# Performance work log

Hardware: AMD Instinct MI355X
Metric: run time of the kernel (lower is better)

The kernel has to match this reference:

```python
import jax, jax.numpy as jnp
import numpy as np

NCLASSES = 80
MAX_BOXES = 100
IOU_THR = 0.5
SCORE_THR = 0.0
NEG = -1e9


def arrange_bbox(xy, wh):
    # xy, wh: [1, H, W, 3, 2]
    H, W = xy.shape[1], xy.shape[2]
    gx, gy = jnp.meshgrid(jnp.arange(W), jnp.arange(H))  # 'xy' indexing, each [H, W]
    grid = jnp.stack([gx, gy], axis=-1)[:, :, None, :].astype(xy.dtype)  # [H, W, 1, 2]
    gsize = jnp.array([H, W], dtype=xy.dtype)  # TF divides last dim [x, y] by [H, W]
    xy = (xy + grid) / gsize
    return jnp.concatenate([xy - wh / 2, xy + wh / 2], axis=-1)  # [1,H,W,3,4]


def hard_nms(boxes, scores):
    # boxes: [N,4] (x1,y1,x2,y2); scores: [N]. Greedy NMS, fixed MAX_BOXES output.
    areas = (boxes[:, 2] - boxes[:, 0]) * (boxes[:, 3] - boxes[:, 1])  # [N]

    def step(sw, _):
        j = jnp.argmax(sw)
        s = sw[j]
        valid = s > SCORE_THR
        bj = boxes[j]
        iw = jnp.clip(jnp.minimum(boxes[:, 2], bj[2]) - jnp.maximum(boxes[:, 0], bj[0]), 0.0)
        ih = jnp.clip(jnp.minimum(boxes[:, 3], bj[3]) - jnp.maximum(boxes[:, 1], bj[1]), 0.0)
        inter = iw * ih
        iou = inter / (areas + areas[j] - inter)
        sw = jnp.where((iou > IOU_THR) & valid, NEG, sw)  # suppresses j itself too
        return sw, (jnp.where(valid, j, -1), jnp.where(valid, s, 0.0), valid)

    _, (sel_idx, sel_scores, valids) = jax.lax.scan(step, scores, None, length=MAX_BOXES)
    return sel_idx, sel_scores, valids


def decode(grid0, grid1, grid2, anchors_table):
    outs = (grid0, grid1, grid2)
    anch = (anchors_table[2], anchors_table[1], anchors_table[0])
    bbs, confs, probs = [], [], []
    for g, a in zip(outs, anch):
        xy, wh, obj, cp = jnp.split(g, [2, 4, 5], axis=-1)
        b = arrange_bbox(xy, jnp.exp(wh) * a)
        bbs.append(b.reshape(1, -1, 4))
        confs.append(obj.reshape(1, -1, 1))
        probs.append(cp.reshape(1, -1, NCLASSES))
    bbox = jnp.concatenate(bbs, axis=1).reshape(-1, 4)          # [N,4]
    conf = jnp.concatenate(confs, axis=1)[0, :, 0]              # [N]
    cp = jnp.concatenate(probs, axis=1)[0]                      # [N,C]
    cls_idx = jnp.argmax(cp, axis=-1)                           # [N]
    maxprob = jnp.max(cp, axis=-1)                              # [N]
    # TF code broadcasts conf[1,N,1]*maxprob[N] -> [N,N], then reduce_max over axis 1.
    # Mathematically: scores[i] = max_j conf[i]*maxprob[j] = max(conf*max(mp), conf*min(mp)).
    scores = jnp.maximum(conf * jnp.max(maxprob), conf * jnp.min(maxprob))
    return bbox, scores, cls_idx


def reference(grid0, grid1, grid2, anchors_table):
    bbox, scores, cls_idx = decode(grid0, grid1, grid2, anchors_table)
    sel_idx, sel_scores, valids = hard_nms(bbox, scores)
    safe = jnp.clip(sel_idx, 0)
    sel_boxes = jnp.where(valids[:, None], bbox[safe], 0.0)[None]      # [1,MAX,4]
    sel_scores = sel_scores[None]                                       # [1,MAX]
    sel_classes = jnp.where(valids, cls_idx[safe], 0)[None]            # [1,MAX]
    num_valid = jnp.sum(valids).astype(jnp.int32)[None]                # [1]
    return sel_boxes, sel_scores, sel_classes, num_valid


def setup_inputs() -> dict:
    key = jax.random.key(0)
    k0, k1, k2 = jax.random.split(key, 3)
    grid0 = jax.random.normal(k0, (1, 48, 48, 3, 85), jnp.float32)
    grid1 = jax.random.normal(k1, (1, 96, 96, 3, 85), jnp.float32)
    grid2 = jax.random.normal(k2, (1, 192, 192, 3, 85), jnp.float32)
    anchors = np.array([[[10, 13], [16, 30], [33, 23]],
                        [[30, 61], [62, 45], [59, 119]],
                        [[116, 90], [156, 198], [373, 326]]], np.float32) / 416.0
    return {"grid0": grid0, "grid1": grid1, "grid2": grid2,
            "anchors_table": jnp.asarray(anchors)}
```

## Files before the change

### kernel.cpp

```cpp
#include <hip/hip_runtime.h>
#include <hip/hip_bf16.h>
#include <math.h>


#define NCLS  80
#define MAXB  100
#define N0    6912
#define N1    27648
#define NTOT  145152
#define NTILE 2268
#define NHB   567
#define NB    4096
#define CAP   2048
#define CAPL  2048
#define NEGF  -3.402823466e38f
#define POSF   3.402823466e38f

#define WS_CONF 0
#define WS_SCAL (NTOT * 4)
#define WS_PART (WS_SCAL + 16)
#define WS_HIST (WS_PART + NTILE * 16)
#define WS_BINC (WS_HIST + 8 * NB * 4)
#define WS_SUF  (WS_BINC + NB * 4)
#define WS_META (WS_SUF + (NB + 4) * 4)
#define WS_CAND (WS_META + 16)

__device__ __forceinline__ int binOf(float s, float Smax) {
    int b = (int)((s / Smax) * (float)NB);
    return b > (NB - 1) ? (NB - 1) : b;
}
__device__ __forceinline__ float rdlane(float v, int l) {
    return __uint_as_float(__builtin_amdgcn_readlane(__float_as_uint(v), l));
}
__device__ __forceinline__ void decodeBox(int idx, const float* __restrict__ g0,
        const float* __restrict__ g1, const float* __restrict__ g2,
        const float* __restrict__ anch,
        float& x1, float& y1, float& x2, float& y2) {
    const float* g; int H, ar, j;
    if (idx < N0)           { g = g0; H = 48;  ar = 2; j = idx; }
    else if (idx < N0 + N1) { g = g1; H = 96;  ar = 1; j = idx - N0; }
    else                    { g = g2; H = 192; ar = 0; j = idx - N0 - N1; }
    const float* r = g + (size_t)j * 85;
    float tx = r[0], ty = r[1], tw = r[2], th = r[3];
    int cell = j / 3, a = j - cell * 3;
    int hh = cell / H, ww = cell - hh * H;
    float xc = (tx + (float)ww) / (float)H;
    float yc = (ty + (float)hh) / (float)H;
    float bw = expf(tw) * anch[ar * 6 + a * 2];
    float bh = expf(th) * anch[ar * 6 + a * 2 + 1];
    x1 = xc - bw * 0.5f; y1 = yc - bh * 0.5f;
    x2 = xc + bw * 0.5f; y2 = yc + bh * 0.5f;
}

__global__ __launch_bounds__(256) void k_decode(
        const float* __restrict__ g0, const float* __restrict__ g1,
        const float* __restrict__ g2, float* __restrict__ conf,
        float* __restrict__ part, int* __restrict__ histAll) {
    __shared__ float sm[5440];
    __shared__ float red[16];
    const int tid = threadIdx.x;
    const int tile = blockIdx.x;
    if (tile < 144) histAll[tile * 256 + tid] = 0;
    const float* p; int ibase, lt;
    if (tile < 108)      { p = g0; ibase = 0;       lt = tile; }
    else if (tile < 540) { p = g1; ibase = N0;      lt = tile - 108; }
    else                 { p = g2; ibase = N0 + N1; lt = tile - 540; }
    const float4* src = (const float4*)(p + (size_t)lt * 5440);
    for (int w = tid; w < 1360; w += 256) ((float4*)sm)[w] = src[w];
    __syncthreads();

    const int b = tid >> 2, pp = tid & 3;
    const float* row = sm + b * 85;
    float best = row[5 + pp * 20];
    #pragma unroll
    for (int k = 1; k < 20; k++) best = fmaxf(best, row[5 + pp * 20 + k]);
    best = fmaxf(best, __shfl_xor(best, 1));
    best = fmaxf(best, __shfl_xor(best, 2));
    float cmx = NEGF, cmn = POSF;
    if (pp == 0) {
        float obj = row[4];
        conf[ibase + lt * 64 + b] = obj;
        cmx = obj; cmn = obj;
    }
    float mpmax = best, mpmin = best;
    for (int off = 32; off; off >>= 1) {
        mpmax = fmaxf(mpmax, __shfl_down(mpmax, off));
        mpmin = fminf(mpmin, __shfl_down(mpmin, off));
        cmx   = fmaxf(cmx,   __shfl_down(cmx,   off));
        cmn   = fminf(cmn,   __shfl_down(cmn,   off));
    }
    const int lane = tid & 63, wid = tid >> 6;
    if (lane == 0) {
        red[wid * 4 + 0] = mpmax; red[wid * 4 + 1] = mpmin;
        red[wid * 4 + 2] = cmx;   red[wid * 4 + 3] = cmn;
    }
    __syncthreads();
    if (tid == 0) {
        float a0 = red[0], a1 = red[1], a2 = red[2], a3 = red[3];
        for (int w = 1; w < 4; w++) {
            a0 = fmaxf(a0, red[w * 4 + 0]); a1 = fminf(a1, red[w * 4 + 1]);
            a2 = fmaxf(a2, red[w * 4 + 2]); a3 = fminf(a3, red[w * 4 + 3]);
        }
        part[tile * 4 + 0] = a0; part[tile * 4 + 1] = a1;
        part[tile * 4 + 2] = a2; part[tile * 4 + 3] = a3;
    }
}

__global__ __launch_bounds__(256) void k_hist(const float* __restrict__ conf,
                                              const float* __restrict__ part,
                                              int* __restrict__ hist) {
    __shared__ float red[16];
    const int tid = threadIdx.x, lane = tid & 63, wid = tid >> 6;
    float a0 = NEGF, a1 = POSF, a2 = NEGF, a3 = POSF;
    for (int b = tid; b < NTILE; b += 256) {
        float4 p4 = ((const float4*)part)[b];
        a0 = fmaxf(a0, p4.x); a1 = fminf(a1, p4.y);
        a2 = fmaxf(a2, p4.z); a3 = fminf(a3, p4.w);
    }
    for (int off = 32; off; off >>= 1) {
        a0 = fmaxf(a0, __shfl_down(a0, off)); a1 = fminf(a1, __shfl_down(a1, off));
        a2 = fmaxf(a2, __shfl_down(a2, off)); a3 = fminf(a3, __shfl_down(a3, off));
    }
    if (lane == 0) {
        red[wid * 4 + 0] = a0; red[wid * 4 + 1] = a1;
        red[wid * 4 + 2] = a2; red[wid * 4 + 3] = a3;
    }
    __syncthreads();
    float Mx = fmaxf(fmaxf(red[0], red[4]),  fmaxf(red[8],  red[12]));
    float Mn = fminf(fminf(red[1], red[5]),  fminf(red[9],  red[13]));
    float cx = fmaxf(fmaxf(red[2], red[6]),  fmaxf(red[10], red[14]));
    float cn = fminf(fminf(red[3], red[7]),  fminf(red[11], red[15]));
    float Smax = fmaxf(fmaxf(cx * Mx, cx * Mn), fmaxf(cn * Mx, cn * Mn));
    int i = blockIdx.x * 256 + tid;
    float c = conf[i];
    float s = fmaxf(c * Mx, c * Mn);
    if (s > 0.0f && Smax > 0.0f)
        atomicAdd(&hist[((blockIdx.x & 7) << 12) + binOf(s, Smax)], 1);
}

__global__ __launch_bounds__(1024) void k_thresh(
        const int* __restrict__ hist, const float* __restrict__ part,
        int* __restrict__ suf, int* __restrict__ meta, float* __restrict__ scal) {
    __shared__ int grp[1024];
    __shared__ int sufL[NB + 1];
    __shared__ float red[64];
    const int tid = threadIdx.x, lane = tid & 63, wid = tid >> 6;
    float a0 = NEGF, a1 = POSF, a2 = NEGF, a3 = POSF;
    for (int b = tid; b < NTILE; b += 1024) {
        float4 p4 = ((const float4*)part)[b];
        a0 = fmaxf(a0, p4.x); a1 = fminf(a1, p4.y);
        a2 = fmaxf(a2, p4.z); a3 = fminf(a3, p4.w);
    }
    for (int off = 32; off; off >>= 1) {
        a0 = fmaxf(a0, __shfl_down(a0, off)); a1 = fminf(a1, __shfl_down(a1, off));
        a2 = fmaxf(a2, __shfl_down(a2, off)); a3 = fminf(a3, __shfl_down(a3, off));
    }
    if (lane == 0) {
        red[wid * 4 + 0] = a0; red[wid * 4 + 1] = a1;
        red[wid * 4 + 2] = a2; red[wid * 4 + 3] = a3;
    }
    int b0 = tid * 4;
    int h[4];
    #pragma unroll
    for (int q = 0; q < 4; q++) {
        int ss = 0;
        #pragma unroll
        for (int sh = 0; sh < 8; sh++) ss += hist[sh * NB + b0 + q];
        h[q] = ss;
    }
    grp[tid] = h[0] + h[1] + h[2] + h[3];
    __syncthreads();
    for (int d = 1; d < 1024; d <<= 1) {
        int add = (tid + d < 1024) ? grp[tid + d] : 0;
        __syncthreads();
        grp[tid] += add;
        __syncthreads();
    }
    int gnext = (tid + 1 < 1024) ? grp[tid + 1] : 0;
    int v3 = gnext + h[3], v2 = v3 + h[2], v1 = v2 + h[1], v0 = v1 + h[0];
    sufL[b0] = v0; sufL[b0 + 1] = v1; sufL[b0 + 2] = v2; sufL[b0 + 3] = v3;
    suf[b0] = v0;  suf[b0 + 1] = v1;  suf[b0 + 2] = v2;  suf[b0 + 3] = v3;
    if (tid == 0) { sufL[NB] = 0; suf[NB] = 0; }
    __syncthreads();
    if (tid < 4) {
        int cap = 256 << tid;
        int L = 0, R = NB - 1, res = NB - 1;
        while (L <= R) {
            int m = (L + R) >> 1;
            if (sufL[m] <= cap) { res = m; R = m - 1; } else L = m + 1;
        }
        meta[tid == 3 ? 0 : tid + 1] = res;
    }
    if (tid == 4) {
        float m0 = red[0], m1 = red[1], m2 = red[2], m3 = red[3];
        for (int w = 1; w < 16; w++) {
            m0 = fmaxf(m0, red[w * 4 + 0]); m1 = fminf(m1, red[w * 4 + 1]);
            m2 = fmaxf(m2, red[w * 4 + 2]); m3 = fminf(m3, red[w * 4 + 3]);
        }
        scal[0] = m0; scal[1] = m1; scal[2] = m2; scal[3] = m3;
    }
}

__global__ __launch_bounds__(256) void k_compact(
        const float* __restrict__ conf, const float* __restrict__ scal,
        const int* __restrict__ suf, const int* __restrict__ meta,
        int* __restrict__ binCtr, unsigned long long* __restrict__ cand) {
    int i = blockIdx.x * 256 + threadIdx.x;
    float Mx = scal[0], Mn = scal[1], cx = scal[2], cn = scal[3];
    float Smax = fmaxf(fmaxf(cx * Mx, cx * Mn), fmaxf(cn * Mx, cn * Mn));
    float c = conf[i];
    float s = fmaxf(c * Mx, c * Mn);
    int lo = meta[0];
    if (s > 0.0f && Smax > 0.0f) {
        int b = binOf(s, Smax);
        if (b >= lo) {
            int pos = suf[b + 1] + atomicAdd(&binCtr[b], 1);
            if (pos < CAP)
                cand[pos] = ((unsigned long long)__float_as_uint(s) << 32)
                          | (unsigned long long)(~(unsigned)i);
        }
    }
}

__global__ __launch_bounds__(64) void k_nms(
        const float* __restrict__ g0, const float* __restrict__ g1,
        const float* __restrict__ g2, const float* __restrict__ anch,
        const float* __restrict__ conf, const float* __restrict__ scal,
        const int* __restrict__ suf, const int* __restrict__ meta,
        const unsigned long long* __restrict__ cand, float* __restrict__ out) {
    __shared__ unsigned long long keys[CAPL];
    __shared__ float selX1[MAXB], selY1[MAXB], selX2[MAXB], selY2[MAXB], selS[MAXB];
    __shared__ int selIdx[MAXB];
    __shared__ int sh_cnt;

    const int lane = threadIdx.x;
    float4 sc4 = *(const float4*)scal;
    const float Mx = sc4.x, Mn = sc4.y;
    const float Smax = fmaxf(fmaxf(sc4.z * Mx, sc4.z * Mn),
                             fmaxf(sc4.w * Mx, sc4.w * Mn));
    int4 mt = *(const int4*)meta;
    int ladMine = 0;
    if (lane == 1) ladMine = mt.y; else if (lane == 2) ladMine = mt.z;
    else if (lane == 3) ladMine = mt.w; else if (lane == 4) ladMine = mt.x;
    int sufMine = (lane >= 1 && lane <= 4) ? suf[ladMine] : 0;
    const int sufA1 = __builtin_amdgcn_readlane(sufMine, 1);
    const int sufA2 = __builtin_amdgcn_readlane(sufMine, 2);
    const int sufA3 = __builtin_amdgcn_readlane(sufMine, 3);
    const int sufA4 = __builtin_amdgcn_readlane(sufMine, 4);

    int nsel = 0;
    float s0x1 = 0, s0y1 = 0, s0x2 = 0, s0y2 = 0, s0a = 0;
    float s1x1 = 0, s1y1 = 0, s1x2 = 0, s1y2 = 0, s1a = 0;

    auto sortDesc = [&](int cnt) {
        int n = 2; while (n < cnt) n <<= 1;
        for (int i = cnt + lane; i < n; i += 64) keys[i] = 0ULL;
        __syncthreads();
        for (int k = 2; k <= n; k <<= 1) {
            for (int j = k >> 1; j > 0; j >>= 1) {
                int half = n >> 1;
                for (int t = lane; t < half; t += 64) {
                    int i = ((t & ~(j - 1)) << 1) | (t & (j - 1));
                    int ixj = i | j;
                    unsigned long long ka = keys[i], kb = keys[ixj];
                    if ((ka < kb) == ((i & k) == 0)) { keys[i] = kb; keys[ixj] = ka; }
                }
                __syncthreads();
            }
        }
    };

    auto sweep = [&](int cnt) {
        for (int bpos = 0; bpos < cnt && nsel < MAXB; bpos += 64) {
            int t = bpos + lane;
            bool alive = (t < cnt);
            float x1 = 0, y1 = 0, x2 = 0, y2 = 0, area = 0, sc = 0;
            int idx = 0;
            if (alive) {
                unsigned long long key = keys[t];
                idx = (int)(~(unsigned)key);
                sc = __uint_as_float((unsigned)(key >> 32));
                decodeBox(idx, g0, g1, g2, anch, x1, y1, x2, y2);
                area = (x2 - x1) * (y2 - y1);
            }
            for (int s2 = 0; s2 < nsel; s2++) {
                float wx1, wy1, wx2, wy2, wa;
                if (s2 < 64) {
                    wx1 = rdlane(s0x1, s2); wy1 = rdlane(s0y1, s2);
                    wx2 = rdlane(s0x2, s2); wy2 = rdlane(s0y2, s2);
                    wa  = rdlane(s0a,  s2);
                } else {
                    int q = s2 - 64;
                    wx1 = rdlane(s1x1, q); wy1 = rdlane(s1y1, q);
                    wx2 = rdlane(s1x2, q); wy2 = rdlane(s1y2, q);
                    wa  = rdlane(s1a,  q);
                }
                if (alive) {
                    float iw = fmaxf(fminf(x2, wx2) - fmaxf(x1, wx1), 0.f);
                    float ih = fmaxf(fminf(y2, wy2) - fmaxf(y1, wy1), 0.f);
                    float inter = iw * ih;
                    if (inter / (area + wa - inter) > 0.5f) alive = false;
                }
            }
            while (nsel < MAXB) {
                unsigned long long bal = __ballot(alive);
                if (!bal) break;
                int w = __ffsll(bal) - 1;
                float wx1 = rdlane(x1, w), wy1 = rdlane(y1, w);
                float wx2 = rdlane(x2, w), wy2 = rdlane(y2, w);
                float wa  = rdlane(area, w);
                if (lane == w) {
                    selX1[nsel] = x1; selY1[nsel] = y1;
                    selX2[nsel] = x2; selY2[nsel] = y2;
                    selS[nsel] = sc; selIdx[nsel] = idx;
                }
                if (nsel < 64) {
                    if (lane == nsel) { s0x1 = wx1; s0y1 = wy1; s0x2 = wx2; s0y2 = wy2; s0a = wa; }
                } else {
                    if (lane == nsel - 64) { s1x1 = wx1; s1y1 = wy1; s1x2 = wx2; s1y2 = wy2; s1a = wa; }
                }
                if (alive) {
                    float iw = fmaxf(fminf(x2, wx2) - fmaxf(x1, wx1), 0.f);
                    float ih = fmaxf(fminf(y2, wy2) - fmaxf(y1, wy1), 0.f);
                    float inter = iw * ih;
                    if (inter / (area + wa - inter) > 0.5f) alive = false;
                }
                nsel++;
            }
        }
    };

    int bases[4] = { 0, sufA1, sufA2, sufA3 };
    int ends[4]  = { sufA1, sufA2, sufA3, sufA4 };
    #pragma unroll
    for (int c = 0; c < 4; c++) {
        if (nsel >= MAXB) break;
        int base = bases[c], cnt = ends[c] - base;
        if (cnt <= 0) continue;
        for (int i = lane; i < cnt; i += 64) keys[i] = cand[base + i];
        sortDesc(cnt);
        sweep(cnt);
    }
    int hi = mt.x, sufHi = sufA4;
    while (nsel < MAXB && hi > 0) {
        int L = 0, R = hi - 1, res = hi - 1, resV = 0;
        while (L <= R) {
            int m = (L + R) >> 1;
            int v = suf[m];
            if (v - sufHi <= CAPL) { res = m; resV = v; R = m - 1; } else L = m + 1;
        }
        int l = res;
        if (lane == 0) sh_cnt = 0;
        __syncthreads();
        for (int i = lane; i < NTOT; i += 64) {
            float c = conf[i];
            float s = fmaxf(c * Mx, c * Mn);
            if (s > 0.0f && Smax > 0.0f) {
                int b = binOf(s, Smax);
                if (b >= l && b < hi) {
                    int pos = atomicAdd(&sh_cnt, 1);
                    if (pos < CAPL)
                        keys[pos] = ((unsigned long long)__float_as_uint(s) << 32)
                                  | (unsigned long long)(~(unsigned)i);
                }
            }
        }
        __syncthreads();
        int cnt = sh_cnt; if (cnt > CAPL) cnt = CAPL;
        if (cnt > 0) { sortDesc(cnt); sweep(cnt); }
        hi = l; sufHi = resV;
    }
    __syncthreads();

    for (int k = lane; k < MAXB; k += 64) {
        float b0 = 0.f, b1 = 0.f, b2 = 0.f, b3 = 0.f, sv = 0.f, cv = 0.f;
        if (k < nsel) {
            b0 = selX1[k]; b1 = selY1[k]; b2 = selX2[k]; b3 = selY2[k];
            sv = selS[k];
            int idx = selIdx[k];
            const float* g; int j;
            if (idx < N0)           { g = g0; j = idx; }
            else if (idx < N0 + N1) { g = g1; j = idx - N0; }
            else                    { g = g2; j = idx - N0 - N1; }
            const float* r = g + (size_t)j * 85 + 5;
            float v[NCLS];
            #pragma unroll
            for (int q = 0; q < NCLS; q++) v[q] = r[q];
            float best = v[0]; int c = 0;
            #pragma unroll
            for (int q = 1; q < NCLS; q++)
                if (v[q] > best) { best = v[q]; c = q; }
            cv = (float)c;
        }
        out[4 * k + 0] = b0; out[4 * k + 1] = b1;
        out[4 * k + 2] = b2; out[4 * k + 3] = b3;
        out[400 + k] = sv;
        out[500 + k] = cv;
    }
    if (lane == 0) out[600] = (float)nsel;
}

extern "C" void kernel_launch(void* const* d_in, const int* in_sizes, int n_in,
                              void* d_out, int out_size, void* d_ws, size_t ws_size,
                              hipStream_t stream) {
    const float* g0   = (const float*)d_in[0];
    const float* g1   = (const float*)d_in[1];
    const float* g2   = (const float*)d_in[2];
    const float* anch = (const float*)d_in[3];
    char* ws = (char*)d_ws;
    float* conf  = (float*)(ws + WS_CONF);
    float* scal  = (float*)(ws + WS_SCAL);
    float* part  = (float*)(ws + WS_PART);
    int*   hist  = (int*)(ws + WS_HIST);
    int*   binc  = (int*)(ws + WS_BINC);
    int*   suf   = (int*)(ws + WS_SUF);
    int*   meta  = (int*)(ws + WS_META);
    unsigned long long* cand = (unsigned long long*)(ws + WS_CAND);
    float* out   = (float*)d_out;

    k_decode <<<NTILE, 256, 0, stream>>>(g0, g1, g2, conf, part, hist);
    k_hist   <<<NHB, 256, 0, stream>>>(conf, part, hist);
    k_thresh <<<1, 1024, 0, stream>>>(hist, part, suf, meta, scal);
    k_compact<<<NHB, 256, 0, stream>>>(conf, scal, suf, meta, binc, cand);
    k_nms    <<<1, 64, 0, stream>>>(g0, g1, g2, anch, conf, scal, suf, meta, cand, out);
}
```

Before: 167.2 us.

## Restructure NMS sweep into per-candidate serial test against lane-held selections

The NMS kernel now decodes all sorted candidate boxes into a shared float4 array up front. It then walks the candidates one at a time, and each lane tests IoU against the one or two selected boxes it holds in registers, with a ballot to decide acceptance. This replaces the old 64-wide batch sweep that used readlane loops and a per-winner serial selection loop. Chunk handling is merged into a single while loop, and the selected score and index are kept in registers instead of shared arrays. The cost is a serial loop over every candidate until 100 are selected, which can mean many more iterations when most candidates are suppressed.

```diff
diff --git a/kernel.cpp b/kernel.cpp
--- a/kernel.cpp
+++ b/kernel.cpp
@@ -28,9 +28,6 @@
 __device__ __forceinline__ int binOf(float s, float Smax) {
     int b = (int)((s / Smax) * (float)NB);
     return b > (NB - 1) ? (NB - 1) : b;
-}
-__device__ __forceinline__ float rdlane(float v, int l) {
-    return __uint_as_float(__builtin_amdgcn_readlane(__float_as_uint(v), l));
 }
 __device__ __forceinline__ void decodeBox(int idx, const float* __restrict__ g0,
         const float* __restrict__ g1, const float* __restrict__ g2,
@@ -229,8 +226,8 @@
         const int* __restrict__ suf, const int* __restrict__ meta,
         const unsigned long long* __restrict__ cand, float* __restrict__ out) {
     __shared__ unsigned long long keys[CAPL];
-    __shared__ float selX1[MAXB], selY1[MAXB], selX2[MAXB], selY2[MAXB], selS[MAXB];
-    __shared__ int selIdx[MAXB];
+    __shared__ float4 bxs[CAPL];
+    __shared__ int lad[5];
     __shared__ int sh_cnt;
 
     const int lane = threadIdx.x;
@@ -243,16 +240,57 @@
     if (lane == 1) ladMine = mt.y; else if (lane == 2) ladMine = mt.z;
     else if (lane == 3) ladMine = mt.w; else if (lane == 4) ladMine = mt.x;
     int sufMine = (lane >= 1 && lane <= 4) ? suf[ladMine] : 0;
-    const int sufA1 = __builtin_amdgcn_readlane(sufMine, 1);
-    const int sufA2 = __builtin_amdgcn_readlane(sufMine, 2);
-    const int sufA3 = __builtin_amdgcn_readlane(sufMine, 3);
-    const int sufA4 = __builtin_amdgcn_readlane(sufMine, 4);
+    if (lane <= 4) lad[lane] = (lane == 0) ? 0 : sufMine;
+    __syncthreads();
+    const int sufA4 = lad[4];
 
     int nsel = 0;
-    float s0x1 = 0, s0y1 = 0, s0x2 = 0, s0y2 = 0, s0a = 0;
-    float s1x1 = 0, s1y1 = 0, s1x2 = 0, s1y2 = 0, s1a = 0;
-
-    auto sortDesc = [&](int cnt) {
+    float s0x1 = 0, s0y1 = 0, s0x2 = 0, s0y2 = 0, s0a = 0, s0s = 0;
+    float s1x1 = 0, s1y1 = 0, s1x2 = 0, s1y2 = 0, s1a = 0, s1s = 0;
+    int s0i = 0, s1i = 0;
+
+    int chunkIdx = 0;
+    int hi = mt.x, sufHi = sufA4;
+
+    while (nsel < MAXB) {
+        int cnt = 0;
+        if (chunkIdx < 4) {
+            int base = lad[chunkIdx], end = lad[chunkIdx + 1];
+            cnt = end - base;
+            for (int i = lane; i < cnt; i += 64) keys[i] = cand[base + i];
+            chunkIdx++;
+            if (cnt <= 0) continue;
+        } else {
+            if (hi <= 0) break;
+            int L = 0, R = hi - 1, res = hi - 1, resV = 0;
+            while (L <= R) {
+                int m = (L + R) >> 1;
+                int v = suf[m];
+                if (v - sufHi <= CAPL) { res = m; resV = v; R = m - 1; } else L = m + 1;
+            }
+            int l = res;
+            if (lane == 0) sh_cnt = 0;
+            __syncthreads();
+            #pragma clang loop unroll(disable)
+            for (int i = lane; i < NTOT; i += 64) {
+                float c = conf[i];
+                float s = fmaxf(c * Mx, c * Mn);
+                if (s > 0.0f && Smax > 0.0f) {
+                    int b = binOf(s, Smax);
+                    if (b >= l && b < hi) {
+                        int pos = atomicAdd(&sh_cnt, 1);
+                        if (pos < CAPL)
+                            keys[pos] = ((unsigned long long)__float_as_uint(s) << 32)
+                                      | (unsigned long long)(~(unsigned)i);
+                    }
+                }
+            }
+            __syncthreads();
+            cnt = sh_cnt; if (cnt > CAPL) cnt = CAPL;
+            hi = l; sufHi = resV;
+            if (cnt <= 0) continue;
+        }
+        __syncthreads();
         int n = 2; while (n < cnt) n <<= 1;
         for (int i = cnt + lane; i < n; i += 64) keys[i] = 0ULL;
         __syncthreads();
@@ -268,134 +306,75 @@
                 __syncthreads();
             }
         }
-    };
-
-    auto sweep = [&](int cnt) {
-        for (int bpos = 0; bpos < cnt && nsel < MAXB; bpos += 64) {
-            int t = bpos + lane;
-            bool alive = (t < cnt);
-            float x1 = 0, y1 = 0, x2 = 0, y2 = 0, area = 0, sc = 0;
-            int idx = 0;
-            if (alive) {
-                unsigned long long key = keys[t];
-                idx = (int)(~(unsigned)key);
-                sc = __uint_as_float((unsigned)(key >> 32));
-                decodeBox(idx, g0, g1, g2, anch, x1, y1, x2, y2);
-                area = (x2 - x1) * (y2 - y1);
-            }
-            for (int s2 = 0; s2 < nsel; s2++) {
-                float wx1, wy1, wx2, wy2, wa;
-                if (s2 < 64) {
-                    wx1 = rdlane(s0x1, s2); wy1 = rdlane(s0y1, s2);
-                    wx2 = rdlane(s0x2, s2); wy2 = rdlane(s0y2, s2);
-                    wa  = rdlane(s0a,  s2);
-                } else {
-                    int q = s2 - 64;
-                    wx1 = rdlane(s1x1, q); wy1 = rdlane(s1y1, q);
-                    wx2 = rdlane(s1x2, q); wy2 = rdlane(s1y2, q);
-                    wa  = rdlane(s1a,  q);
-                }
-                if (alive) {
-                    float iw = fmaxf(fminf(x2, wx2) - fmaxf(x1, wx1), 0.f);
-                    float ih = fmaxf(fminf(y2, wy2) - fmaxf(y1, wy1), 0.f);
-                    float inter = iw * ih;
-                    if (inter / (area + wa - inter) > 0.5f) alive = false;
-                }
-            }
-            while (nsel < MAXB) {
-                unsigned long long bal = __ballot(alive);
-                if (!bal) break;
-                int w = __ffsll(bal) - 1;
-                float wx1 = rdlane(x1, w), wy1 = rdlane(y1, w);
-                float wx2 = rdlane(x2, w), wy2 = rdlane(y2, w);
-                float wa  = rdlane(area, w);
-                if (lane == w) {
-                    selX1[nsel] = x1; selY1[nsel] = y1;
-                    selX2[nsel] = x2; selY2[nsel] = y2;
-                    selS[nsel] = sc; selIdx[nsel] = idx;
-                }
-                if (nsel < 64) {
-                    if (lane == nsel) { s0x1 = wx1; s0y1 = wy1; s0x2 = wx2; s0y2 = wy2; s0a = wa; }
-                } else {
-                    if (lane == nsel - 64) { s1x1 = wx1; s1y1 = wy1; s1x2 = wx2; s1y2 = wy2; s1a = wa; }
-                }
-                if (alive) {
-                    float iw = fmaxf(fminf(x2, wx2) - fmaxf(x1, wx1), 0.f);
-                    float ih = fmaxf(fminf(y2, wy2) - fmaxf(y1, wy1), 0.f);
-                    float inter = iw * ih;
-                    if (inter / (area + wa - inter) > 0.5f) alive = false;
+        for (int t = lane; t < cnt; t += 64) {
+            int idx = (int)(~(unsigned)keys[t]);
+            float x1, y1, x2, y2;
+            decodeBox(idx, g0, g1, g2, anch, x1, y1, x2, y2);
+            bxs[t] = make_float4(x1, y1, x2, y2);
+        }
+        __syncthreads();
+        for (int c2 = 0; c2 < cnt && nsel < MAXB; c2++) {
+            unsigned long long key = keys[c2];
+            float4 cb = bxs[c2];
+            float ca = (cb.z - cb.x) * (cb.w - cb.y);
+            bool sup = false;
+            if (lane < nsel) {
+                float iw = fmaxf(fminf(cb.z, s0x2) - fmaxf(cb.x, s0x1), 0.f);
+                float ih = fmaxf(fminf(cb.w, s0y2) - fmaxf(cb.y, s0y1), 0.f);
+                float inter = iw * ih;
+                sup = inter / (ca + s0a - inter) > 0.5f;
+            }
+            if (lane + 64 < nsel) {
+                float iw = fmaxf(fminf(cb.z, s1x2) - fmaxf(cb.x, s1x1), 0.f);
+                float ih = fmaxf(fminf(cb.w, s1y2) - fmaxf(cb.y, s1y1), 0.f);
+                float inter = iw * ih;
+                sup |= inter / (ca + s1a - inter) > 0.5f;
+            }
+            if (__ballot(sup) == 0ULL) {
+                if (lane == nsel) {
+                    s0x1 = cb.x; s0y1 = cb.y; s0x2 = cb.z; s0y2 = cb.w; s0a = ca;
+                    s0s = __uint_as_float((unsigned)(key >> 32));
+                    s0i = (int)(~(unsigned)key);
+                } else if (lane == nsel - 64) {
+                    s1x1 = cb.x; s1y1 = cb.y; s1x2 = cb.z; s1y2 = cb.w; s1a = ca;
+                    s1s = __uint_as_float((unsigned)(key >> 32));
+                    s1i = (int)(~(unsigned)key);
                 }
                 nsel++;
             }
         }
-    };
-
-    int bases[4] = { 0, sufA1, sufA2, sufA3 };
-    int ends[4]  = { sufA1, sufA2, sufA3, sufA4 };
-    #pragma unroll
-    for (int c = 0; c < 4; c++) {
-        if (nsel >= MAXB) break;
-        int base = bases[c], cnt = ends[c] - base;
-        if (cnt <= 0) continue;
-        for (int i = lane; i < cnt; i += 64) keys[i] = cand[base + i];
-        sortDesc(cnt);
-        sweep(cnt);
-    }
-    int hi = mt.x, sufHi = sufA4;
-    while (nsel < MAXB && hi > 0) {
-        int L = 0, R = hi - 1, res = hi - 1, resV = 0;
-        while (L <= R) {
-            int m = (L + R) >> 1;
-            int v = suf[m];
-            if (v - sufHi <= CAPL) { res = m; resV = v; R = m - 1; } else L = m + 1;
-        }
-        int l = res;
-        if (lane == 0) sh_cnt = 0;
-        __syncthreads();
-        for (int i = lane; i < NTOT; i += 64) {
-            float c = conf[i];
-            float s = fmaxf(c * Mx, c * Mn);
-            if (s > 0.0f && Smax > 0.0f) {
-                int b = binOf(s, Smax);
-                if (b >= l && b < hi) {
-                    int pos = atomicAdd(&sh_cnt, 1);
-                    if (pos < CAPL)
-                        keys[pos] = ((unsigned long long)__float_as_uint(s) << 32)
-                                  | (unsigned long long)(~(unsigned)i);
-                }
-            }
-        }
-        __syncthreads();
-        int cnt = sh_cnt; if (cnt > CAPL) cnt = CAPL;
-        if (cnt > 0) { sortDesc(cnt); sweep(cnt); }
-        hi = l; sufHi = resV;
-    }
-    __syncthreads();
-
-    for (int k = lane; k < MAXB; k += 64) {
-        float b0 = 0.f, b1 = 0.f, b2 = 0.f, b3 = 0.f, sv = 0.f, cv = 0.f;
-        if (k < nsel) {
-            b0 = selX1[k]; b1 = selY1[k]; b2 = selX2[k]; b3 = selY2[k];
-            sv = selS[k];
-            int idx = selIdx[k];
+    }
+
+    for (int set = 0; set < 2; set++) {
+        int k = lane + (set << 6);
+        bool valid = (k < nsel) && (k < MAXB);
+        float ox1 = set ? s1x1 : s0x1, oy1 = set ? s1y1 : s0y1;
+        float ox2 = set ? s1x2 : s0x2, oy2 = set ? s1y2 : s0y2;
+        float osc = set ? s1s : s0s;
+        int   oi  = set ? s1i : s0i;
+        float cv = 0.f;
+        if (valid) {
             const float* g; int j;
-            if (idx < N0)           { g = g0; j = idx; }
-            else if (idx < N0 + N1) { g = g1; j = idx - N0; }
-            else                    { g = g2; j = idx - N0 - N1; }
+            if (oi < N0)           { g = g0; j = oi; }
+            else if (oi < N0 + N1) { g = g1; j = oi - N0; }
+            else                   { g = g2; j = oi - N0 - N1; }
             const float* r = g + (size_t)j * 85 + 5;
-            float v[NCLS];
-            #pragma unroll
-            for (int q = 0; q < NCLS; q++) v[q] = r[q];
-            float best = v[0]; int c = 0;
-            #pragma unroll
-            for (int q = 1; q < NCLS; q++)
-                if (v[q] > best) { best = v[q]; c = q; }
+            float best = NEGF; int c = 0;
+            #pragma unroll 8
+            for (int q = 0; q < NCLS; q++) {
+                float v = r[q];
+                if (v > best) { best = v; c = q; }
+            }
             cv = (float)c;
         }
-        out[4 * k + 0] = b0; out[4 * k + 1] = b1;
-        out[4 * k + 2] = b2; out[4 * k + 3] = b3;
-        out[400 + k] = sv;
-        out[500 + k] = cv;
+        if (k < MAXB) {
+            out[4 * k + 0] = valid ? ox1 : 0.f;
+            out[4 * k + 1] = valid ? oy1 : 0.f;
+            out[4 * k + 2] = valid ? ox2 : 0.f;
+            out[4 * k + 3] = valid ? oy2 : 0.f;
+            out[400 + k] = valid ? osc : 0.f;
+            out[500 + k] = cv;
+        }
     }
     if (lane == 0) out[600] = (float)nsel;
 }
```

New measurement: 164.4 us. No clear change (-1.7%).
